# Performance work log

Hardware: AMD Instinct MI355X
Metric: run time of the kernel (lower is better)

## Reference

```python
import jax, jax.numpy as jnp
import numpy as np

B, T, D = 2, 2048, 2048
HK, HV, K, V = 16, 32, 128, 128          # key heads, value heads, head dims
KEY_DIM, VALUE_DIM = HK * K, HV * V      # 2048, 4096
CONV_W = 4                               # causal conv kernel width
EPS = 1e-6


def setup_inputs() -> dict:
    key = jax.random.key(0)
    ks = jax.random.split(key, 8)
    rn = lambda k, shp, sc: jax.random.normal(k, shp, dtype=jnp.float32) * sc
    return {
        "hidden_states": rn(ks[0], (B, T, D), 1.0),
        "W_qkvz": rn(ks[1], (D, 2 * KEY_DIM + 2 * VALUE_DIM), D ** -0.5),
        "W_ba": rn(ks[2], (D, 2 * HV), D ** -0.5),
        "conv_weight": rn(ks[3], (2 * KEY_DIM + VALUE_DIM, CONV_W), CONV_W ** -0.5),
        "A_log": jnp.log(jax.random.uniform(ks[4], (HV,), minval=1.0, maxval=16.0)),
        "dt_bias": rn(ks[5], (HV,), 0.5),
        "norm_weight": jnp.zeros((V,), jnp.float32),  # zero-centered RMSNorm weight
        "W_out": rn(ks[6], (VALUE_DIM, D), VALUE_DIM ** -0.5),
    }


def _l2norm(x):
    return x * jax.lax.rsqrt(jnp.sum(x * x, axis=-1, keepdims=True) + 1e-6)


def _causal_conv_silu(x, w):
    # x: [B,T,C]; depthwise causal conv, kernel width CONV_W, then SiLU
    xp = jnp.pad(x, ((0, 0), (CONV_W - 1, 0), (0, 0)))
    out = sum(xp[:, j:j + x.shape[1], :] * w[None, None, :, j] for j in range(CONV_W))
    return jax.nn.silu(out)


def _gated_delta_rule(q, k, v, g, beta):
    # q,k: [B,T,HV,K] (l2-normed, q pre-scaled); v: [B,T,HV,V]; g,beta: [B,T,HV]
    def step(S, xs):                      # S: [B,HV,K,V]
        q_t, k_t, v_t, g_t, beta_t = xs
        S = S * jnp.exp(g_t)[..., None, None]
        pred = jnp.einsum('bhk,bhkv->bhv', k_t, S)
        delta = (v_t - pred) * beta_t[..., None]
        S = S + jnp.einsum('bhk,bhv->bhkv', k_t, delta)
        o_t = jnp.einsum('bhk,bhkv->bhv', q_t, S)
        return S, o_t

    mv = lambda x: jnp.moveaxis(x, 1, 0)  # time-major for scan
    S0 = jnp.zeros((q.shape[0], HV, K, V), q.dtype)
    _, o = jax.lax.scan(step, S0, (mv(q), mv(k), mv(v), mv(g), mv(beta)))
    return jnp.moveaxis(o, 0, 1)          # [B,T,HV,V]


def reference(hidden_states, W_qkvz, W_ba, conv_weight, A_log, dt_bias,
              norm_weight, W_out):
    b_, t_ = hidden_states.shape[:2]
    qkvz = hidden_states @ W_qkvz
    q, k, v, z = jnp.split(qkvz, [KEY_DIM, 2 * KEY_DIM, 2 * KEY_DIM + VALUE_DIM], axis=-1)
    ba = hidden_states @ W_ba
    b_gate, a = jnp.split(ba, 2, axis=-1)  # each [B,T,HV]

    # fused causal conv1d + SiLU over concat(q,k,v)
    mixed = _causal_conv_silu(jnp.concatenate([q, k, v], axis=-1), conv_weight)
    q, k, v = jnp.split(mixed, [KEY_DIM, 2 * KEY_DIM], axis=-1)

    # gating: beta = sigmoid(b), g = -exp(A_log) * softplus(a + dt_bias)
    beta = jax.nn.sigmoid(b_gate)
    g = -jnp.exp(A_log) * jax.nn.softplus(a + dt_bias)

    # GQA expand (v_per_k_group = HV // HK), l2norm, scale
    rep = HV // HK
    q = jnp.repeat(q.reshape(b_, t_, HK, K), rep, axis=2)
    k = jnp.repeat(k.reshape(b_, t_, HK, K), rep, axis=2)
    v = v.reshape(b_, t_, HV, V)
    q = _l2norm(q) * (K ** -0.5)
    k = _l2norm(k)

    o = _gated_delta_rule(q, k, v, g, beta)  # [B,T,HV,V]

    # gated RMSNorm (per value head, zero-centered weight) then out projection
    zg = z.reshape(b_, t_, HV, V)
    x = o * jax.nn.silu(zg)
    var = jnp.mean(x * x, axis=-1, keepdims=True)
    x = x * jax.lax.rsqrt(var + EPS) * (1.0 + norm_weight)
    return x.reshape(b_, t_, VALUE_DIM) @ W_out
```

## Files before the change

### kernel.cpp

```cpp
#include <hip/hip_runtime.h>

typedef unsigned short u16;
typedef unsigned int u32;

typedef short bf16x8 __attribute__((ext_vector_type(8)));
typedef float f32x4 __attribute__((ext_vector_type(4)));
typedef float f32x16 __attribute__((ext_vector_type(16)));

#define T_SEQ 2048
#define MFMA16(a, b, c) __builtin_amdgcn_mfma_f32_16x16x32_bf16(a, b, c, 0, 0, 0)
#define MFMA32(a, b, c) __builtin_amdgcn_mfma_f32_32x32x16_bf16(a, b, c, 0, 0, 0)

__device__ __forceinline__ u16 f2bf(float f) {
    u32 u = __float_as_uint(f);
    u += 0x7fffu + ((u >> 16) & 1u);
    return (u16)(u >> 16);
}
__device__ __forceinline__ float bf2f(u16 s) {
    return __uint_as_float(((u32)s) << 16);
}
__device__ __forceinline__ void g2lds16(const u16* gp, u16* lp) {
    __builtin_amdgcn_global_load_lds((const __attribute__((address_space(1))) void*)gp,
                                     (__attribute__((address_space(3))) void*)lp, 16, 0, 0);
}

__global__ __launch_bounds__(256) void cast_f32_bf16(const float* __restrict__ in,
                                                     u16* __restrict__ out, long n) {
    long i = ((long)blockIdx.x * 256 + threadIdx.x) * 4;
    if (i + 3 < n) {
        float4 v = *(const float4*)&in[i];
        out[i + 0] = f2bf(v.x);
        out[i + 1] = f2bf(v.y);
        out[i + 2] = f2bf(v.z);
        out[i + 3] = f2bf(v.w);
    }
}

__global__ __launch_bounds__(256) void transpose_cast(const float* __restrict__ in,
                                                      u16* __restrict__ out, int R, int C) {
    __shared__ float tile[32][33];
    int c0 = blockIdx.x * 32, r0 = blockIdx.y * 32;
    int tx = threadIdx.x & 31, ty = threadIdx.x >> 5;
#pragma unroll
    for (int rr = 0; rr < 32; rr += 8)
        tile[ty + rr][tx] = in[(long)(r0 + ty + rr) * C + c0 + tx];
    __syncthreads();
#pragma unroll
    for (int rr = 0; rr < 32; rr += 8)
        out[(long)(c0 + ty + rr) * R + r0 + tx] = f2bf(tile[tx][ty + rr]);
}

template <int MODE>
__global__ __launch_bounds__(256) void gemm_bt(const u16* __restrict__ A,
                                               const u16* __restrict__ B, void* __restrict__ C,
                                               void* __restrict__ C2, int M, int N, int K, int lda,
                                               int ldb, int ldc) {
    __shared__ __align__(16) u16 As[128 * 32];
    __shared__ __align__(16) u16 Bs[128 * 32];
    int m0 = blockIdx.x * 128, n0 = blockIdx.y * 128;
    int tid = threadIdx.x;
    int lane = tid & 63, w = tid >> 6;
    int wr = w >> 1, wc = w & 1;
    int l31 = lane & 31, hf = lane >> 5;

    f32x16 acc[2][2];
#pragma unroll
    for (int mi = 0; mi < 2; mi++)
#pragma unroll
        for (int nj = 0; nj < 2; nj++)
#pragma unroll
            for (int r = 0; r < 16; r++) acc[mi][nj][r] = 0.f;

    int srow = tid >> 2, sc8 = (tid & 3) * 8;
    const u16* Ag = &A[(long)(m0 + srow) * lda + sc8];
    const u16* Bg = &B[(long)(n0 + srow) * ldb + sc8];

    for (int k0 = 0; k0 < K; k0 += 32) {
        g2lds16(Ag + k0, &As[tid * 8]);
        g2lds16(Ag + (long)64 * lda + k0, &As[(256 + tid) * 8]);
        g2lds16(Bg + k0, &Bs[tid * 8]);
        g2lds16(Bg + (long)64 * ldb + k0, &Bs[(256 + tid) * 8]);
        __syncthreads();
        bf16x8 af[2][2], bfr[2][2];
#pragma unroll
        for (int mi = 0; mi < 2; mi++)
#pragma unroll
            for (int ks = 0; ks < 2; ks++) {
                af[mi][ks] = *(const bf16x8*)&As[(wr * 64 + mi * 32 + l31) * 32 + ks * 16 + hf * 8];
                bfr[mi][ks] =
                    *(const bf16x8*)&Bs[(wc * 64 + mi * 32 + l31) * 32 + ks * 16 + hf * 8];
            }
#pragma unroll
        for (int ks = 0; ks < 2; ks++)
#pragma unroll
            for (int mi = 0; mi < 2; mi++)
#pragma unroll
                for (int nj = 0; nj < 2; nj++)
                    acc[mi][nj] = MFMA32(af[mi][ks], bfr[nj][ks], acc[mi][nj]);
        __syncthreads();
    }

    if (MODE == 0) {
#pragma unroll
        for (int mi = 0; mi < 2; mi++)
#pragma unroll
            for (int nj = 0; nj < 2; nj++)
#pragma unroll
                for (int r = 0; r < 16; r++) {
                    int row = m0 + wr * 64 + mi * 32 + (r >> 2) * 8 + hf * 4 + (r & 3);
                    int col = n0 + wc * 64 + nj * 32 + l31;
                    ((float*)C)[(long)row * ldc + col] = acc[mi][nj][r];
                }
    } else {
        u16* dst;
        long dldc;
        int ncol0;
        if (MODE == 2 && n0 >= 8192) {
            dst = (u16*)C2;
            dldc = 4096;
            ncol0 = n0 - 8192;
        } else {
            dst = (u16*)C;
            dldc = (MODE == 2) ? 8192 : ldc;
            ncol0 = n0;
        }
#pragma unroll 1
        for (int half_e = 0; half_e < 2; half_e++) {
            __syncthreads();
            if (wc == half_e) {
#pragma unroll
                for (int mi = 0; mi < 2; mi++)
#pragma unroll
                    for (int nj = 0; nj < 2; nj++)
#pragma unroll
                        for (int r = 0; r < 16; r++) {
                            int row = wr * 64 + mi * 32 + (r >> 2) * 8 + hf * 4 + (r & 3);
                            int col = nj * 32 + l31;
                            u16* base = (row < 64) ? As : Bs;
                            base[(row & 63) * 64 + col] = f2bf(acc[mi][nj][r]);
                        }
            }
            __syncthreads();
#pragma unroll
            for (int rr = 0; rr < 4; rr++) {
                int row = rr * 32 + (tid >> 3), seg = tid & 7;
                u16* base = (row < 64) ? As : Bs;
                *(uint4*)&dst[(long)(m0 + row) * dldc + ncol0 + half_e * 64 + seg * 8] =
                    *(uint4*)&base[(row & 63) * 64 + seg * 8];
            }
        }
    }
}

__global__ __launch_bounds__(256) void ba_gemm(const u16* __restrict__ hid,
                                               const u16* __restrict__ WbaT,
                                               const float* __restrict__ A_log,
                                               const float* __restrict__ dt_bias,
                                               float* __restrict__ g, float* __restrict__ beta) {
    __shared__ __align__(16) u16 As2[32 * 32];
    __shared__ __align__(16) u16 Bs2[64 * 32];
    int m0 = blockIdx.x * 32;
    int tid = threadIdx.x, lane = tid & 63, w = tid >> 6;
    int quad = lane >> 4, l15 = lane & 15;
    int trow = w & 1;
    int ctile = (w >> 1) * 2;
    f32x4 acc[2];
    acc[0] = (f32x4){0.f, 0.f, 0.f, 0.f};
    acc[1] = (f32x4){0.f, 0.f, 0.f, 0.f};
    int srow = tid >> 2, sc8 = (tid & 3) * 8;
    for (int k0 = 0; k0 < 2048; k0 += 32) {
        if (tid < 128)
            *(uint4*)&As2[srow * 32 + sc8] = *(const uint4*)&hid[(long)(m0 + srow) * 2048 + k0 + sc8];
        *(uint4*)&Bs2[srow * 32 + sc8] = *(const uint4*)&WbaT[(long)srow * 2048 + k0 + sc8];
        __syncthreads();
        bf16x8 a = *(const bf16x8*)&As2[(trow * 16 + l15) * 32 + quad * 8];
#pragma unroll
        for (int j = 0; j < 2; j++) {
            bf16x8 b = *(const bf16x8*)&Bs2[((ctile + j) * 16 + l15) * 32 + quad * 8];
            acc[j] = MFMA16(a, b, acc[j]);
        }
        __syncthreads();
    }
#pragma unroll
    for (int j = 0; j < 2; j++)
#pragma unroll
        for (int r = 0; r < 4; r++) {
            int tok = m0 + trow * 16 + quad * 4 + r;
            int col = (ctile + j) * 16 + l15;
            float tot = acc[j][r];
            if (col < 32) {
                beta[(long)tok * 32 + col] = 1.f / (1.f + expf(-tot));
            } else {
                int h = col - 32;
                float x = tot + dt_bias[h];
                float sp = (x > 20.f) ? x : log1pf(expf(x));
                g[(long)tok * 32 + h] = -expf(A_log[h]) * sp;
            }
        }
}

__global__ __launch_bounds__(256) void conv_gate(const u16* __restrict__ qkv,
                                                 const float* __restrict__ conv_w,
                                                 u16* __restrict__ qn, u16* __restrict__ kn,
                                                 u16* __restrict__ vc) {
    int tok = blockIdx.x, tid = threadIdx.x;
    int tloc = tok & (T_SEQ - 1);
    __shared__ float mixed[8192];
    __shared__ float sh_norm[32];
    uint4 zero4;
    zero4.x = zero4.y = zero4.z = zero4.w = 0u;
#pragma unroll
    for (int i = 0; i < 4; i++) {
        int c = (i * 256 + tid) * 8;
        long base = (long)tok * 8192 + c;
        uint4 x3 = *(const uint4*)&qkv[base];
        uint4 x2 = (tloc >= 1) ? *(const uint4*)&qkv[base - 8192] : zero4;
        uint4 x1 = (tloc >= 2) ? *(const uint4*)&qkv[base - 16384] : zero4;
        uint4 x0 = (tloc >= 3) ? *(const uint4*)&qkv[base - 24576] : zero4;
        const u16* p0 = (const u16*)&x0;
        const u16* p1 = (const u16*)&x1;
        const u16* p2 = (const u16*)&x2;
        const u16* p3 = (const u16*)&x3;
#pragma unroll
        for (int e = 0; e < 8; e++) {
            float4 wv = *(const float4*)&conv_w[(long)(c + e) * 4];
            float a = bf2f(p0[e]) * wv.x + bf2f(p1[e]) * wv.y + bf2f(p2[e]) * wv.z +
                      bf2f(p3[e]) * wv.w;
            mixed[c + e] = a / (1.f + __expf(-a));
        }
    }
    __syncthreads();
    int grp = tid >> 3, sub = tid & 7;
    float ss = 0.f;
#pragma unroll
    for (int e = 0; e < 16; e++) {
        float v = mixed[grp * 128 + sub * 16 + e];
        ss += v * v;
    }
    ss += __shfl_xor(ss, 4, 8);
    ss += __shfl_xor(ss, 2, 8);
    ss += __shfl_xor(ss, 1, 8);
    if (sub == 0) sh_norm[grp] = rsqrtf(ss + 1e-6f);
    __syncthreads();
#pragma unroll
    for (int i = 0; i < 4; i++) {
        int c = (i * 256 + tid) * 8;
        float nf = (c < 2048) ? sh_norm[c >> 7] * 0.08838834764831845f
                              : ((c < 4096) ? sh_norm[c >> 7] : 1.f);
        u16 ob[8];
#pragma unroll
        for (int e = 0; e < 8; e++) ob[e] = f2bf(mixed[c + e] * nf);
        uint4 val = *(uint4*)ob;
        if (c < 2048)
            *(uint4*)&qn[(long)tok * 2048 + c] = val;
        else if (c < 4096)
            *(uint4*)&kn[(long)tok * 2048 + (c - 2048)] = val;
        else
            *(uint4*)&vc[(long)tok * 4096 + (c - 4096)] = val;
    }
}

__global__ __launch_bounds__(256) void phaseA(const u16* __restrict__ qn,
                                              const u16* __restrict__ kn,
                                              const u16* __restrict__ vc,
                                              const float* __restrict__ g,
                                              const float* __restrict__ beta,
                                              u16* __restrict__ Tv_g, u16* __restrict__ Tw_g,
                                              u16* __restrict__ Q2_g, u16* __restrict__ obuf) {
    __shared__ __align__(16) u16 Yrm[64][256];
    __shared__ __align__(16) float BMt[64][64];
    __shared__ __align__(16) u16 kbuf[64][128];
    u16* Lbf = &kbuf[0][0];

    int bid = blockIdx.x;
    int c = bid & 31, h = (bid >> 5) & 31, b = bid >> 10;
    int hk = h >> 1;
    long tokbase = (long)b * T_SEQ + c * 64;
    long cb = (long)bid * 8192;
    int tid = threadIdx.x, lane = tid & 63, w = tid >> 6;
    int quad = lane >> 4, l15 = lane & 15;

    float gl = g[(tokbase + lane) * 32 + h];
    float bl = beta[(tokbase + lane) * 32 + h];
    float cgl = gl;
#pragma unroll
    for (int d = 1; d < 64; d <<= 1) {
        float y = __shfl_up(cgl, d);
        if (lane >= d) cgl += y;
    }
    float wscl = bl * __expf(cgl);
    float eCgl = __expf(cgl);

#pragma unroll
    for (int p = 0; p < 4; p++) {
        int u = p * 256 + tid;
        int row = u >> 4, col8 = (u & 15) * 8;
        *(uint4*)&kbuf[row][col8] = *(const uint4*)&kn[(tokbase + row) * 2048 + hk * 128 + col8];
    }
    __syncthreads();

    {
        f32x4 gk[4];
#pragma unroll
        for (int nj = 0; nj < 4; nj++) gk[nj] = (f32x4){0.f, 0.f, 0.f, 0.f};
#pragma unroll
        for (int kk = 0; kk < 4; kk++) {
            bf16x8 a = *(const bf16x8*)&kbuf[w * 16 + l15][kk * 32 + quad * 8];
#pragma unroll
            for (int nj = 0; nj < 4; nj++) {
                bf16x8 bb = *(const bf16x8*)&kbuf[nj * 16 + l15][kk * 32 + quad * 8];
                gk[nj] = MFMA16(a, bb, gk[nj]);
            }
        }
#pragma unroll
        for (int nj = 0; nj < 4; nj++)
#pragma unroll
            for (int r = 0; r < 4; r++) {
                int i = w * 16 + quad * 4 + r;
                int j = nj * 16 + l15;
                float cgi = __shfl(cgl, i), cgj = __shfl(cgl, j);
                float bi = __shfl(bl, i);
                BMt[j][i] = (j < i) ? bi * gk[nj][r] * __expf(cgi - cgj) : 0.f;
            }
    }
    __syncthreads();

    {
        int col = tid;
        bool isV = col < 128;
        int kcol = col & 127;
        long vbase = tokbase * 4096 + h * 128 + kcol;
        float Yreg[8], acc8[8];
#pragma unroll 1
        for (int bi = 0; bi < 8; ++bi) {
            float vr[8];
            if (isV) {
#pragma unroll
                for (int ii = 0; ii < 8; ii++)
                    vr[ii] = bf2f(vc[vbase + (long)(bi * 8 + ii) * 4096]);
            }
#pragma unroll
            for (int ii = 0; ii < 8; ii++) acc8[ii] = 0.f;
            for (int j = 0; j < bi * 8; ++j) {
                float yv = bf2f(Yrm[j][col]);
                float4 m0 = *(const float4*)&BMt[j][bi * 8];
                float4 m1 = *(const float4*)&BMt[j][bi * 8 + 4];
                acc8[0] += m0.x * yv;
                acc8[1] += m0.y * yv;
                acc8[2] += m0.z * yv;
                acc8[3] += m0.w * yv;
                acc8[4] += m1.x * yv;
                acc8[5] += m1.y * yv;
                acc8[6] += m1.z * yv;
                acc8[7] += m1.w * yv;
            }
#pragma unroll
            for (int ii = 0; ii < 8; ii++) {
                int i = bi * 8 + ii;
                float rhs = isV ? __shfl(bl, i) * vr[ii] : __shfl(wscl, i) * bf2f(kbuf[i][kcol]);
                float s = rhs - acc8[ii];
#pragma unroll
                for (int jj = 0; jj < 8; jj++)
                    if (jj < ii) s -= BMt[bi * 8 + jj][i] * Yreg[jj];
                Yreg[ii] = s;
                u16 sb = f2bf(s);
                Yrm[i][col] = sb;
                if (isV)
                    Tv_g[cb + i * 128 + kcol] = sb;
                else
                    Tw_g[cb + i * 128 + kcol] = sb;
            }
        }
    }
    __syncthreads();

    {
        f32x4 qk_[4];
#pragma unroll
        for (int nj = 0; nj < 4; nj++) qk_[nj] = (f32x4){0.f, 0.f, 0.f, 0.f};
#pragma unroll
        for (int kk = 0; kk < 4; kk++) {
            bf16x8 a = *(const bf16x8*)&qn[(tokbase + w * 16 + l15) * 2048 + hk * 128 + kk * 32 +
                                           quad * 8];
#pragma unroll
            for (int nj = 0; nj < 4; nj++) {
                bf16x8 bb = *(const bf16x8*)&kbuf[nj * 16 + l15][kk * 32 + quad * 8];
                qk_[nj] = MFMA16(a, bb, qk_[nj]);
            }
        }
        __syncthreads();
#pragma unroll
        for (int nj = 0; nj < 4; nj++)
#pragma unroll
            for (int r = 0; r < 4; r++) {
                int t = w * 16 + quad * 4 + r;
                int rr = nj * 16 + l15;
                float cgt = __shfl(cgl, t), cgr = __shfl(cgl, rr);
                float val = (rr <= t) ? qk_[nj][r] * __expf(cgt - cgr) : 0.f;
                Lbf[t * 64 + rr] = f2bf(val);
            }
    }
    __syncthreads();

#pragma unroll 1
    for (int half = 0; half < 2; half++) {
        f32x4 oa[8];
#pragma unroll
        for (int nj = 0; nj < 8; nj++) oa[nj] = (f32x4){0.f, 0.f, 0.f, 0.f};
#pragma unroll
        for (int kk = 0; kk < 2; kk++) {
            bf16x8 a = *(const bf16x8*)&Lbf[(w * 16 + l15) * 64 + kk * 32 + quad * 8];
#pragma unroll
            for (int nj = 0; nj < 8; nj++) {
                bf16x8 bb;
#pragma unroll
                for (int jj = 0; jj < 8; jj++)
                    bb[jj] = (short)Yrm[kk * 32 + quad * 8 + jj][half * 128 + nj * 16 + l15];
                oa[nj] = MFMA16(a, bb, oa[nj]);
            }
        }
        if (half == 0) {
#pragma unroll
            for (int nj = 0; nj < 8; nj++)
#pragma unroll
                for (int r = 0; r < 4; r++) {
                    int t = w * 16 + quad * 4 + r;
                    int vcol = nj * 16 + l15;
                    obuf[(tokbase + t) * 4096 + h * 128 + vcol] = f2bf(oa[nj][r]);
                }
        } else {
#pragma unroll
            for (int nj = 0; nj < 8; nj++)
#pragma unroll
                for (int r = 0; r < 4; r++) {
                    int t = w * 16 + quad * 4 + r;
                    int kcol = nj * 16 + l15;
                    float qsc = __shfl(eCgl, t);
                    float qv = bf2f(qn[(tokbase + t) * 2048 + hk * 128 + kcol]);
                    Q2_g[cb + t * 128 + kcol] = f2bf(qsc * qv - oa[nj][r]);
                }
        }
    }
}

__global__ __launch_bounds__(256) void phaseB(const u16* __restrict__ kn,
                                              const float* __restrict__ g,
                                              const u16* __restrict__ Tv_g,
                                              const u16* __restrict__ Tw_g,
                                              const u16* __restrict__ Q2_g,
                                              u16* __restrict__ obuf) {
    __shared__ __align__(16) float Sf[128][32];
    __shared__ __align__(16) u16 SbfT[32][136];
    __shared__ __align__(16) u16 KhT[128][72];
    __shared__ __align__(16) u16 Ut[32][72];

    int bid = blockIdx.x;
    int vq = bid & 3, h = (bid >> 2) & 31, b = bid >> 7;
    int hk = h >> 1;
    int tid = threadIdx.x, lane = tid & 63, w = tid >> 6;
    int quad = lane >> 4, l15 = lane & 15;

    for (int p = tid; p < 128 * 32; p += 256) ((float*)Sf)[p] = 0.f;
    for (int p = tid; p < 32 * 136; p += 256) ((u16*)SbfT)[p] = 0;
    __syncthreads();

    float gl_pf;
    uint4 kreg[4];
    bf16x8 aTw[4], aQ2[4];
    u16 tvv_pf[2][4], oold[2][4];

#define PB_PREFETCH(cc)                                                                      \
    {                                                                                        \
        long tb_ = (long)b * T_SEQ + (cc) * 64;                                              \
        long cb_ = ((long)((b * 32 + h) * 32) + (cc)) * 8192;                                \
        gl_pf = g[(tb_ + lane) * 32 + h];                                                    \
        const u16* kp_ = &kn[(tb_ + lane) * 2048 + hk * 128 + w * 32];                       \
        kreg[0] = *(const uint4*)&kp_[0];                                                    \
        kreg[1] = *(const uint4*)&kp_[8];                                                    \
        kreg[2] = *(const uint4*)&kp_[16];                                                   \
        kreg[3] = *(const uint4*)&kp_[24];                                                   \
        _Pragma("unroll") for (int kk = 0; kk < 4; kk++) {                                   \
            aTw[kk] = *(const bf16x8*)&Tw_g[cb_ + (w * 16 + l15) * 128 + kk * 32 + quad * 8]; \
            aQ2[kk] = *(const bf16x8*)&Q2_g[cb_ + (w * 16 + l15) * 128 + kk * 32 + quad * 8]; \
        }                                                                                    \
        _Pragma("unroll") for (int nj = 0; nj < 2; nj++) _Pragma("unroll")                   \
            for (int r = 0; r < 4; r++) {                                                    \
            int i_ = w * 16 + quad * 4 + r;                                                  \
            int vg_ = vq * 32 + nj * 16 + l15;                                               \
            tvv_pf[nj][r] = Tv_g[cb_ + (long)i_ * 128 + vg_];                                \
            oold[nj][r] = obuf[(tb_ + i_) * 4096 + h * 128 + vg_];                           \
        }                                                                                    \
    }

    PB_PREFETCH(0);

    for (int c = 0; c < 32; ++c) {
        long tokbase = (long)b * T_SEQ + c * 64;
        float cgl = gl_pf;
#pragma unroll
        for (int d = 1; d < 64; d <<= 1) {
            float y = __shfl_up(cgl, d);
            if (lane >= d) cgl += y;
        }
        float cgC = __shfl(cgl, 63);
        float A_C = __expf(cgC);
        float kscl = __expf(cgC - cgl);

        {
            const u16* kk16 = (const u16*)kreg;
#pragma unroll
            for (int j = 0; j < 32; j++) KhT[w * 32 + j][lane] = f2bf(bf2f(kk16[j]) * kscl);
        }

        f32x4 y1[2], oo[2];
#pragma unroll
        for (int nj = 0; nj < 2; nj++) {
            y1[nj] = (f32x4){0.f, 0.f, 0.f, 0.f};
            oo[nj] = (f32x4){0.f, 0.f, 0.f, 0.f};
        }
#pragma unroll
        for (int kk = 0; kk < 4; kk++) {
#pragma unroll
            for (int nj = 0; nj < 2; nj++) {
                bf16x8 bb = *(const bf16x8*)&SbfT[nj * 16 + l15][kk * 32 + quad * 8];
                y1[nj] = MFMA16(aTw[kk], bb, y1[nj]);
                oo[nj] = MFMA16(aQ2[kk], bb, oo[nj]);
            }
        }
#pragma unroll
        for (int nj = 0; nj < 2; nj++)
#pragma unroll
            for (int r = 0; r < 4; r++) {
                int i = w * 16 + quad * 4 + r;
                int vl = nj * 16 + l15;
                int vg = vq * 32 + vl;
                Ut[vl][i] = f2bf(bf2f(tvv_pf[nj][r]) - y1[nj][r]);
                obuf[(tokbase + i) * 4096 + h * 128 + vg] =
                    f2bf(bf2f(oold[nj][r]) + oo[nj][r]);
            }
        __syncthreads();

        if (c + 1 < 32) PB_PREFETCH(c + 1);

#pragma unroll
        for (int mm = 0; mm < 2; mm++) {
            int mi = 2 * w + mm;
#pragma unroll
            for (int nj = 0; nj < 2; nj++) {
                f32x4 sacc;
#pragma unroll
                for (int r = 0; r < 4; r++)
                    sacc[r] = A_C * Sf[mi * 16 + quad * 4 + r][nj * 16 + l15];
#pragma unroll
                for (int kk = 0; kk < 2; kk++) {
                    bf16x8 a = *(const bf16x8*)&KhT[mi * 16 + l15][kk * 32 + quad * 8];
                    bf16x8 bb = *(const bf16x8*)&Ut[nj * 16 + l15][kk * 32 + quad * 8];
                    sacc = MFMA16(a, bb, sacc);
                }
#pragma unroll
                for (int r = 0; r < 4; r++) {
                    int kd = mi * 16 + quad * 4 + r, vl = nj * 16 + l15;
                    Sf[kd][vl] = sacc[r];
                    SbfT[vl][kd] = f2bf(sacc[r]);
                }
            }
        }
        __syncthreads();
    }
#undef PB_PREFETCH
}

__global__ __launch_bounds__(256) void gated_norm(const u16* __restrict__ obuf,
                                                  const u16* __restrict__ zbuf,
                                                  const float* __restrict__ norm_w,
                                                  u16* __restrict__ xn) {
    int tok = blockIdx.x, tid = threadIdx.x;
    long obase = (long)tok * 4096 + tid * 16;
    u16 ob[16], zb[16];
    *(uint4*)(ob + 0) = *(const uint4*)&obuf[obase];
    *(uint4*)(ob + 8) = *(const uint4*)&obuf[obase + 8];
    *(uint4*)(zb + 0) = *(const uint4*)&zbuf[obase];
    *(uint4*)(zb + 8) = *(const uint4*)&zbuf[obase + 8];
    float x[16];
    float ss = 0.f;
#pragma unroll
    for (int i = 0; i < 16; i++) {
        float ov = bf2f(ob[i]);
        float zv = bf2f(zb[i]);
        float xv = ov * (zv / (1.f + expf(-zv)));
        x[i] = xv;
        ss += xv * xv;
    }
    ss += __shfl_xor(ss, 4, 8);
    ss += __shfl_xor(ss, 2, 8);
    ss += __shfl_xor(ss, 1, 8);
    float scale = rsqrtf(ss * (1.f / 128.f) + 1e-6f);
    int cbase = (tid * 16) & 127;
#pragma unroll
    for (int i = 0; i < 16; i++)
        xn[(long)tok * 4096 + tid * 16 + i] = f2bf(x[i] * scale * (1.f + norm_w[cbase + i]));
}

extern "C" void kernel_launch(void* const* d_in, const int* in_sizes, int n_in, void* d_out,
                              int out_size, void* d_ws, size_t ws_size, hipStream_t stream) {
    const float* hidden = (const float*)d_in[0];
    const float* W_qkvz = (const float*)d_in[1];
    const float* W_ba = (const float*)d_in[2];
    const float* conv_w = (const float*)d_in[3];
    const float* A_log = (const float*)d_in[4];
    const float* dt_bias = (const float*)d_in[5];
    const float* norm_w = (const float*)d_in[6];
    const float* W_out = (const float*)d_in[7];
    float* out = (float*)d_out;

    char* ws = (char*)d_ws;
    u16* wqT = (u16*)(ws + 0);
    u16* qn = (u16*)(ws + 0);
    u16* vc = (u16*)(ws + 16777216L);
    u16* hidbf = (u16*)(ws + 50331648L);
    u16* kn = (u16*)(ws + 50331648L);
    u16* woT = (u16*)(ws + 67108864L);
    u16* qkv_raw = (u16*)(ws + 83886080L);
    u16* Tv = (u16*)(ws + 83886080L);
    u16* Tw = (u16*)(ws + 117440512L);
    u16* xn = (u16*)(ws + 83886080L);
    u16* WbaT = (u16*)(ws + 150994944L);
    u16* zbuf = (u16*)(ws + 150994944L);
    u16* Q2 = (u16*)(ws + 184549376L);
    float* g = (float*)(ws + 218103808L);
    float* beta = (float*)(ws + 218628096L);
    u16* obuf = vc;

    cast_f32_bf16<<<8192, 256, 0, stream>>>(hidden, hidbf, 8388608L);
    transpose_cast<<<dim3(384, 64), 256, 0, stream>>>(W_qkvz, wqT, 2048, 12288);
    transpose_cast<<<dim3(64, 128), 256, 0, stream>>>(W_out, woT, 4096, 2048);
    transpose_cast<<<dim3(2, 64), 256, 0, stream>>>(W_ba, WbaT, 2048, 64);
    ba_gemm<<<128, 256, 0, stream>>>(hidbf, WbaT, A_log, dt_bias, g, beta);
    gemm_bt<2><<<dim3(32, 96), 256, 0, stream>>>(hidbf, wqT, qkv_raw, zbuf, 4096, 12288, 2048,
                                                 2048, 2048, 0);
    conv_gate<<<4096, 256, 0, stream>>>(qkv_raw, conv_w, qn, kn, vc);
    phaseA<<<2048, 256, 0, stream>>>(qn, kn, vc, g, beta, Tv, Tw, Q2, obuf);
    phaseB<<<256, 256, 0, stream>>>(kn, g, Tv, Tw, Q2, obuf);
    gated_norm<<<4096, 256, 0, stream>>>(obuf, zbuf, norm_w, xn);
    gemm_bt<0><<<dim3(32, 16), 256, 0, stream>>>(xn, woT, out, nullptr, 4096, 2048, 4096, 4096,
                                                 4096, 2048);
}
```

Baseline: 1.038 ms.

## Swizzle and pad LDS tiles, transpose Y buffer, register-resident conv normalization

Applies an XOR swizzle to the main GEMM's LDS tiles and pads the ba_gemm and chunk-kernel LDS arrays, to cut bank conflicts. Stores the solved Y matrix transposed, so MFMA B-operands load as one 16-byte vector instead of eight scalar gathers. Rewrites conv_gate so each thread keeps 32 channels in registers and computes the per-head L2 norm with a 4-lane shuffle, removing the shared buffer and two barriers. Padding raises LDS use and the new conv layout changes global access coalescing.

```diff
diff --git a/kernel.cpp b/kernel.cpp
--- a/kernel.cpp
+++ b/kernel.cpp
@@ -62,6 +62,7 @@
     int lane = tid & 63, w = tid >> 6;
     int wr = w >> 1, wc = w & 1;
     int l31 = lane & 31, hf = lane >> 5;
+    int swz = (l31 >> 1) & 3;
 
     f32x16 acc[2][2];
 #pragma unroll
@@ -71,7 +72,8 @@
 #pragma unroll
             for (int r = 0; r < 16; r++) acc[mi][nj][r] = 0.f;
 
-    int srow = tid >> 2, sc8 = (tid & 3) * 8;
+    int srow = tid >> 2;
+    int sc8 = (((tid & 3) ^ ((srow >> 1) & 3))) * 8;
     const u16* Ag = &A[(long)(m0 + srow) * lda + sc8];
     const u16* Bg = &B[(long)(n0 + srow) * ldb + sc8];
 
@@ -86,9 +88,9 @@
         for (int mi = 0; mi < 2; mi++)
 #pragma unroll
             for (int ks = 0; ks < 2; ks++) {
-                af[mi][ks] = *(const bf16x8*)&As[(wr * 64 + mi * 32 + l31) * 32 + ks * 16 + hf * 8];
-                bfr[mi][ks] =
-                    *(const bf16x8*)&Bs[(wc * 64 + mi * 32 + l31) * 32 + ks * 16 + hf * 8];
+                int cellA = ((ks * 2 + hf) ^ swz) * 8;
+                af[mi][ks] = *(const bf16x8*)&As[(wr * 64 + mi * 32 + l31) * 32 + cellA];
+                bfr[mi][ks] = *(const bf16x8*)&Bs[(wc * 64 + mi * 32 + l31) * 32 + cellA];
             }
 #pragma unroll
         for (int ks = 0; ks < 2; ks++)
@@ -157,8 +159,8 @@
                                                const float* __restrict__ A_log,
                                                const float* __restrict__ dt_bias,
                                                float* __restrict__ g, float* __restrict__ beta) {
-    __shared__ __align__(16) u16 As2[32 * 32];
-    __shared__ __align__(16) u16 Bs2[64 * 32];
+    __shared__ __align__(16) u16 As2[32 * 40];
+    __shared__ __align__(16) u16 Bs2[64 * 40];
     int m0 = blockIdx.x * 32;
     int tid = threadIdx.x, lane = tid & 63, w = tid >> 6;
     int quad = lane >> 4, l15 = lane & 15;
@@ -170,13 +172,14 @@
     int srow = tid >> 2, sc8 = (tid & 3) * 8;
     for (int k0 = 0; k0 < 2048; k0 += 32) {
         if (tid < 128)
-            *(uint4*)&As2[srow * 32 + sc8] = *(const uint4*)&hid[(long)(m0 + srow) * 2048 + k0 + sc8];
-        *(uint4*)&Bs2[srow * 32 + sc8] = *(const uint4*)&WbaT[(long)srow * 2048 + k0 + sc8];
+            *(uint4*)&As2[srow * 40 + sc8] =
+                *(const uint4*)&hid[(long)(m0 + srow) * 2048 + k0 + sc8];
+        *(uint4*)&Bs2[srow * 40 + sc8] = *(const uint4*)&WbaT[(long)srow * 2048 + k0 + sc8];
         __syncthreads();
-        bf16x8 a = *(const bf16x8*)&As2[(trow * 16 + l15) * 32 + quad * 8];
+        bf16x8 a = *(const bf16x8*)&As2[(trow * 16 + l15) * 40 + quad * 8];
 #pragma unroll
         for (int j = 0; j < 2; j++) {
-            bf16x8 b = *(const bf16x8*)&Bs2[((ctile + j) * 16 + l15) * 32 + quad * 8];
+            bf16x8 b = *(const bf16x8*)&Bs2[((ctile + j) * 16 + l15) * 40 + quad * 8];
             acc[j] = MFMA16(a, b, acc[j]);
         }
         __syncthreads();
@@ -205,55 +208,50 @@
                                                  u16* __restrict__ vc) {
     int tok = blockIdx.x, tid = threadIdx.x;
     int tloc = tok & (T_SEQ - 1);
-    __shared__ float mixed[8192];
-    __shared__ float sh_norm[32];
+    int c0 = tid * 32;
+    long base = (long)tok * 8192 + c0;
+    float mx[32];
     uint4 zero4;
     zero4.x = zero4.y = zero4.z = zero4.w = 0u;
 #pragma unroll
-    for (int i = 0; i < 4; i++) {
-        int c = (i * 256 + tid) * 8;
-        long base = (long)tok * 8192 + c;
-        uint4 x3 = *(const uint4*)&qkv[base];
-        uint4 x2 = (tloc >= 1) ? *(const uint4*)&qkv[base - 8192] : zero4;
-        uint4 x1 = (tloc >= 2) ? *(const uint4*)&qkv[base - 16384] : zero4;
-        uint4 x0 = (tloc >= 3) ? *(const uint4*)&qkv[base - 24576] : zero4;
+    for (int e8 = 0; e8 < 4; e8++) {
+        long b8 = base + e8 * 8;
+        uint4 x3 = *(const uint4*)&qkv[b8];
+        uint4 x2 = (tloc >= 1) ? *(const uint4*)&qkv[b8 - 8192] : zero4;
+        uint4 x1 = (tloc >= 2) ? *(const uint4*)&qkv[b8 - 16384] : zero4;
+        uint4 x0 = (tloc >= 3) ? *(const uint4*)&qkv[b8 - 24576] : zero4;
         const u16* p0 = (const u16*)&x0;
         const u16* p1 = (const u16*)&x1;
         const u16* p2 = (const u16*)&x2;
         const u16* p3 = (const u16*)&x3;
 #pragma unroll
         for (int e = 0; e < 8; e++) {
-            float4 wv = *(const float4*)&conv_w[(long)(c + e) * 4];
+            float4 wv = *(const float4*)&conv_w[(long)(c0 + e8 * 8 + e) * 4];
             float a = bf2f(p0[e]) * wv.x + bf2f(p1[e]) * wv.y + bf2f(p2[e]) * wv.z +
                       bf2f(p3[e]) * wv.w;
-            mixed[c + e] = a / (1.f + __expf(-a));
-        }
-    }
-    __syncthreads();
-    int grp = tid >> 3, sub = tid & 7;
-    float ss = 0.f;
-#pragma unroll
-    for (int e = 0; e < 16; e++) {
-        float v = mixed[grp * 128 + sub * 16 + e];
-        ss += v * v;
-    }
-    ss += __shfl_xor(ss, 4, 8);
-    ss += __shfl_xor(ss, 2, 8);
-    ss += __shfl_xor(ss, 1, 8);
-    if (sub == 0) sh_norm[grp] = rsqrtf(ss + 1e-6f);
-    __syncthreads();
-#pragma unroll
-    for (int i = 0; i < 4; i++) {
-        int c = (i * 256 + tid) * 8;
-        float nf = (c < 2048) ? sh_norm[c >> 7] * 0.08838834764831845f
-                              : ((c < 4096) ? sh_norm[c >> 7] : 1.f);
+            mx[e8 * 8 + e] = a / (1.f + __expf(-a));
+        }
+    }
+    float nf = 1.f;
+    if (c0 < 4096) {
+        float ss = 0.f;
+#pragma unroll
+        for (int e = 0; e < 32; e++) ss += mx[e] * mx[e];
+        ss += __shfl_xor(ss, 1, 4);
+        ss += __shfl_xor(ss, 2, 4);
+        nf = rsqrtf(ss + 1e-6f);
+        if (c0 < 2048) nf *= 0.08838834764831845f;
+    }
+#pragma unroll
+    for (int e8 = 0; e8 < 4; e8++) {
         u16 ob[8];
 #pragma unroll
-        for (int e = 0; e < 8; e++) ob[e] = f2bf(mixed[c + e] * nf);
+        for (int e = 0; e < 8; e++) ob[e] = f2bf(mx[e8 * 8 + e] * nf);
         uint4 val = *(uint4*)ob;
-        if (c < 2048)
+        int c = c0 + e8 * 8;
+        if (c0 < 2048)
             *(uint4*)&qn[(long)tok * 2048 + c] = val;
-        else if (c < 4096)
+        else if (c0 < 4096)
             *(uint4*)&kn[(long)tok * 2048 + (c - 2048)] = val;
         else
             *(uint4*)&vc[(long)tok * 4096 + (c - 4096)] = val;
@@ -267,9 +265,9 @@
                                               const float* __restrict__ beta,
                                               u16* __restrict__ Tv_g, u16* __restrict__ Tw_g,
                                               u16* __restrict__ Q2_g, u16* __restrict__ obuf) {
-    __shared__ __align__(16) u16 Yrm[64][256];
-    __shared__ __align__(16) float BMt[64][64];
-    __shared__ __align__(16) u16 kbuf[64][128];
+    __shared__ __align__(16) u16 kbuf[64][136];
+    __shared__ __align__(16) float BMt[64][68];
+    __shared__ __align__(16) u16 YT[256][72];
     u16* Lbf = &kbuf[0][0];
 
     int bid = blockIdx.x;
@@ -342,7 +340,7 @@
 #pragma unroll
             for (int ii = 0; ii < 8; ii++) acc8[ii] = 0.f;
             for (int j = 0; j < bi * 8; ++j) {
-                float yv = bf2f(Yrm[j][col]);
+                float yv = bf2f(YT[col][j]);
                 float4 m0 = *(const float4*)&BMt[j][bi * 8];
                 float4 m1 = *(const float4*)&BMt[j][bi * 8 + 4];
                 acc8[0] += m0.x * yv;
@@ -354,6 +352,7 @@
                 acc8[6] += m1.z * yv;
                 acc8[7] += m1.w * yv;
             }
+            u16 outb[8];
 #pragma unroll
             for (int ii = 0; ii < 8; ii++) {
                 int i = bi * 8 + ii;
@@ -363,12 +362,15 @@
                 for (int jj = 0; jj < 8; jj++)
                     if (jj < ii) s -= BMt[bi * 8 + jj][i] * Yreg[jj];
                 Yreg[ii] = s;
-                u16 sb = f2bf(s);
-                Yrm[i][col] = sb;
+                outb[ii] = f2bf(s);
+            }
+            *(uint4*)&YT[col][bi * 8] = *(uint4*)outb;
+#pragma unroll
+            for (int ii = 0; ii < 8; ii++) {
                 if (isV)
-                    Tv_g[cb + i * 128 + kcol] = sb;
+                    Tv_g[cb + (bi * 8 + ii) * 128 + kcol] = outb[ii];
                 else
-                    Tw_g[cb + i * 128 + kcol] = sb;
+                    Tw_g[cb + (bi * 8 + ii) * 128 + kcol] = outb[ii];
             }
         }
     }
@@ -397,7 +399,7 @@
                 int rr = nj * 16 + l15;
                 float cgt = __shfl(cgl, t), cgr = __shfl(cgl, rr);
                 float val = (rr <= t) ? qk_[nj][r] * __expf(cgt - cgr) : 0.f;
-                Lbf[t * 64 + rr] = f2bf(val);
+                Lbf[t * 72 + rr] = f2bf(val);
             }
     }
     __syncthreads();
@@ -409,13 +411,10 @@
         for (int nj = 0; nj < 8; nj++) oa[nj] = (f32x4){0.f, 0.f, 0.f, 0.f};
 #pragma unroll
         for (int kk = 0; kk < 2; kk++) {
-            bf16x8 a = *(const bf16x8*)&Lbf[(w * 16 + l15) * 64 + kk * 32 + quad * 8];
+            bf16x8 a = *(const bf16x8*)&Lbf[(w * 16 + l15) * 72 + kk * 32 + quad * 8];
 #pragma unroll
             for (int nj = 0; nj < 8; nj++) {
-                bf16x8 bb;
-#pragma unroll
-                for (int jj = 0; jj < 8; jj++)
-                    bb[jj] = (short)Yrm[kk * 32 + quad * 8 + jj][half * 128 + nj * 16 + l15];
+                bf16x8 bb = *(const bf16x8*)&YT[half * 128 + nj * 16 + l15][kk * 32 + quad * 8];
                 oa[nj] = MFMA16(a, bb, oa[nj]);
             }
         }
@@ -535,8 +534,7 @@
                 int vl = nj * 16 + l15;
                 int vg = vq * 32 + vl;
                 Ut[vl][i] = f2bf(bf2f(tvv_pf[nj][r]) - y1[nj][r]);
-                obuf[(tokbase + i) * 4096 + h * 128 + vg] =
-                    f2bf(bf2f(oold[nj][r]) + oo[nj][r]);
+                obuf[(tokbase + i) * 4096 + h * 128 + vg] = f2bf(bf2f(oold[nj][r]) + oo[nj][r]);
             }
         __syncthreads();
 
```

Measured after the change: 1.090 ms. 5.0% more time.
